# Kernel tuning notes

Measured on AMD Instinct MI355X. Metric: run time of the kernel, lower is better.

The kernel has to match this reference:

```python
import jax, jax.numpy as jnp
import numpy as np

B, C, T = 512, 256, 256
E, K, G = 8, 5, 8
EPS = 1e-5


def setup_inputs() -> dict:
    key = jax.random.key(0)
    k1, k2, k3, k4 = jax.random.split(key, 4)
    x = jax.random.normal(k1, (B, C, T), dtype=jnp.float32)
    use_expert_i = jax.random.randint(k2, (B,), 0, E, dtype=jnp.int32)
    # per-expert Conv1d params: weight [E, Cout, Cin, K], bias [E, Cout]
    W = jax.random.normal(k3, (E, C, C, K), dtype=jnp.float32) * 0.05
    b = jax.random.normal(k4, (E, C), dtype=jnp.float32) * 0.05
    # per-expert GroupNorm affine params (torch default init: gamma=1, beta=0)
    gamma = jnp.ones((E, C), dtype=jnp.float32)
    beta = jnp.zeros((E, C), dtype=jnp.float32)
    return {"x": x, "use_expert_i": use_expert_i, "W": W, "b": b,
            "gamma": gamma, "beta": beta}


def _mish(y):
    return y * jnp.tanh(jax.nn.softplus(y))


def reference(x, use_expert_i, W, b, gamma, beta):
    # Top-1 one-hot routing => weight is exactly 1 for the selected expert, so
    # output[b] = Mish(GroupNorm(Conv1d_{e_b}(x[b]))). Gather per-sample params
    # instead of looping over experts (same math, vectorized).
    pad = K // 2
    Wb = W[use_expert_i]        # [B, Cout, Cin, K]
    bb = b[use_expert_i]        # [B, Cout]
    gb = gamma[use_expert_i]    # [B, Cout]
    betab = beta[use_expert_i]  # [B, Cout]

    def per_sample_conv(xi, wi, bi):
        # xi: [Cin, T], wi: [Cout, Cin, K] -> [Cout, T] ('same' padding)
        y = jax.lax.conv_general_dilated(xi[None], wi, window_strides=(1,),
                                         padding=[(pad, pad)])[0]
        return y + bi[:, None]

    y = jax.vmap(per_sample_conv)(x, Wb, bb)  # [B, C, T]

    # GroupNorm: normalize over (channels-in-group, length) per sample
    yg = y.reshape(B, G, C // G, T)
    mu = jnp.mean(yg, axis=(2, 3), keepdims=True)
    var = jnp.var(yg, axis=(2, 3), keepdims=True)
    yn = ((yg - mu) * jax.lax.rsqrt(var + EPS)).reshape(B, C, T)
    yn = yn * gb[:, :, None] + betab[:, :, None]
    return _mish(yn)
```

## Files before the change

kernel.cpp:

```cpp
#include <hip/hip_runtime.h>
#include <cmath>

constexpr int Bn = 512, Cn = 256, Tn = 256, En = 8;
constexpr float EPSf = 1e-5f;

using bf16x8 = __attribute__((ext_vector_type(8))) short;
using f32x4  = __attribute__((ext_vector_type(4))) float;

__device__ __forceinline__ ushort f2bf(float f) {
    uint u = __builtin_bit_cast(uint, f);
    uint r = u + 0x7FFFu + ((u >> 16) & 1u);
    return (ushort)(r >> 16);
}

__global__ __launch_bounds__(256)
void wconv_kernel(const float* __restrict__ Wf, ushort* __restrict__ Wws) {
    int idx = blockIdx.x * 256 + threadIdx.x;
    const float* src = Wf + (size_t)idx * 5;
    int ci = idx & 255, co = (idx >> 8) & 255, e = idx >> 16;
#pragma unroll
    for (int k = 0; k < 5; ++k)
        Wws[(((size_t)(e * 5 + k) * 256 + co) << 8) + ci] = f2bf(src[k]);
}

__global__ __launch_bounds__(256)
void xpose_kernel(const float* __restrict__ x, ushort* __restrict__ xT) {
    const int id = blockIdx.x;
    const int b  = id >> 5;
    const int cc = (id >> 3) & 3, tc = id & 7;
    const int ci0 = cc * 64, t0 = tc * 32;
    const int tid = threadIdx.x;

    __shared__ float ls[64][33];

    const int tl = tid & 31;
#pragma unroll
    for (int jj = 0; jj < 8; ++jj) {
        const int cil = (tid >> 5) * 8 + jj;
        ls[cil][tl] = x[((size_t)(b * 256 + ci0 + cil)) * 256 + t0 + tl];
    }
    __syncthreads();

    const int ciw = tid & 63;
#pragma unroll
    for (int jj = 0; jj < 8; ++jj) {
        const int tw = (tid >> 6) * 8 + jj;
        xT[((size_t)(b * 256 + t0 + tw)) * 256 + ci0 + ciw] = f2bf(ls[ciw][tw]);
    }
}

template<int MODE>
__global__ __launch_bounds__(256, 3)
void conv_gn_mish(const float* __restrict__ x, const ushort* __restrict__ xTw,
                  const int* __restrict__ expert,
                  const float* __restrict__ Wf, const ushort* __restrict__ Wws,
                  const float* __restrict__ bias, const float* __restrict__ gamma,
                  const float* __restrict__ beta, float* __restrict__ out)
{
    const int id = blockIdx.x;
    const int wg = (id & 7) * 256 + (id >> 3);
    const int b  = wg >> 2;
    const int gp = wg & 3;
    const int cb = gp * 64;
    const int e  = __builtin_amdgcn_readfirstlane(expert[b]);

    const int tid = threadIdx.x;
    const int w = tid >> 6, l = tid & 63, q = l >> 4, r = l & 15;

    __shared__ ushort xT[2][260 * 40];
    __shared__ float red[4][4];

    f32x4 acc[4][4];
#pragma unroll
    for (int m = 0; m < 4; ++m)
#pragma unroll
        for (int n = 0; n < 4; ++n) acc[m][n] = f32x4{0.f, 0.f, 0.f, 0.f};

    if (tid < 8) {
        const int bf = tid >> 2, rr = tid & 3;
        const int row = (rr < 2) ? rr : (256 + rr);
#pragma unroll
        for (int i = 0; i < 10; ++i)
            *reinterpret_cast<uint2*>(&xT[bf][row * 40 + i * 4]) = make_uint2(0u, 0u);
    }

    bf16x8 g[4];
    float v[4][8];

#define STAGE_LOAD(CI0) {                                                    \
        if (MODE == 2) {                                                     \
            const ushort* xb = xTw + ((size_t)b * 256) * 256 + (CI0) + w * 8;\
            _Pragma("unroll")                                                \
            for (int tt = 0; tt < 4; ++tt)                                   \
                g[tt] = *reinterpret_cast<const bf16x8*>(                    \
                    xb + (size_t)(tt * 64 + l) * 256);                       \
        } else {                                                             \
            const float* xb = x + ((size_t)b * Cn + (CI0) + w * 8) * Tn;     \
            _Pragma("unroll")                                                \
            for (int tt = 0; tt < 4; ++tt) {                                 \
                const int t = tt * 64 + l;                                   \
                _Pragma("unroll")                                            \
                for (int rr = 0; rr < 8; ++rr) v[tt][rr] = xb[rr * Tn + t];  \
            }                                                                \
        }                                                                    \
    }
#define STAGE_WRITE(BUF) {                                                   \
        ushort* dst = xT[BUF];                                               \
        if (MODE == 2) {                                                     \
            _Pragma("unroll")                                                \
            for (int tt = 0; tt < 4; ++tt)                                   \
                *reinterpret_cast<bf16x8*>(                                  \
                    &dst[(tt * 64 + l + 2) * 40 + w * 8]) = g[tt];           \
        } else {                                                             \
            _Pragma("unroll")                                                \
            for (int tt = 0; tt < 4; ++tt) {                                 \
                const int t = tt * 64 + l;                                   \
                uint p0 = (uint)f2bf(v[tt][0]) | ((uint)f2bf(v[tt][1]) << 16); \
                uint p1 = (uint)f2bf(v[tt][2]) | ((uint)f2bf(v[tt][3]) << 16); \
                uint p2 = (uint)f2bf(v[tt][4]) | ((uint)f2bf(v[tt][5]) << 16); \
                uint p3 = (uint)f2bf(v[tt][6]) | ((uint)f2bf(v[tt][7]) << 16); \
                *reinterpret_cast<uint2*>(&dst[(t + 2) * 40 + w * 8])     = make_uint2(p0, p1); \
                *reinterpret_cast<uint2*>(&dst[(t + 2) * 40 + w * 8 + 4]) = make_uint2(p2, p3); \
            }                                                                \
        }                                                                    \
    }

    STAGE_LOAD(0);
    STAGE_WRITE(0);
    STAGE_LOAD(32);
    __syncthreads();

#pragma unroll 1
    for (int ct = 0; ct < 8; ++ct) {
        if (ct < 7) {
            STAGE_WRITE((ct + 1) & 1);
            if (ct < 6) STAGE_LOAD((ct + 2) * 32);
        }
        const int ci0 = ct * 32;
        const ushort* src = xT[ct & 1];

#pragma unroll
        for (int k = 0; k < 5; ++k) {
            bf16x8 A[4];
#pragma unroll
            for (int m = 0; m < 4; ++m) {
                if (MODE >= 1) {
                    A[m] = *reinterpret_cast<const bf16x8*>(
                        Wws + (((size_t)((e * 5 + k) * 256 + cb + m * 16 + r)) << 8)
                            + ci0 + q * 8);
                } else {
                    bf16x8 a;
#pragma unroll
                    for (int j = 0; j < 8; ++j)
                        a[j] = (short)f2bf(
                            Wf[((size_t)(e * 256 + cb + m * 16 + r) * 256
                                + ci0 + q * 8 + j) * 5 + k]);
                    A[m] = a;
                }
            }
#pragma unroll
            for (int n = 0; n < 4; ++n) {
                const bf16x8 Bf = *reinterpret_cast<const bf16x8*>(
                    &src[(w * 64 + n * 16 + r + k) * 40 + q * 8]);
#pragma unroll
                for (int m = 0; m < 4; ++m)
                    acc[m][n] = __builtin_amdgcn_mfma_f32_16x16x32_bf16(
                        A[m], Bf, acc[m][n], 0, 0, 0);
            }
        }
        __syncthreads();
    }
#undef STAGE_LOAD
#undef STAGE_WRITE

    float s1a = 0.f, s2a = 0.f, s1b = 0.f, s2b = 0.f;
#pragma unroll
    for (int m = 0; m < 4; ++m) {
#pragma unroll
        for (int i = 0; i < 4; ++i) {
            const float bv = bias[e * Cn + cb + m * 16 + q * 4 + i];
#pragma unroll
            for (int n = 0; n < 4; ++n) {
                const float val = acc[m][n][i] + bv;
                acc[m][n][i] = val;
                if (m < 2) { s1a += val; s2a += val * val; }
                else       { s1b += val; s2b += val * val; }
            }
        }
    }
#pragma unroll
    for (int off = 32; off; off >>= 1) {
        s1a += __shfl_xor(s1a, off); s2a += __shfl_xor(s2a, off);
        s1b += __shfl_xor(s1b, off); s2b += __shfl_xor(s2b, off);
    }
    if (l == 0) { red[w][0] = s1a; red[w][1] = s2a; red[w][2] = s1b; red[w][3] = s2b; }
    __syncthreads();
    const float S1a = red[0][0] + red[1][0] + red[2][0] + red[3][0];
    const float S2a = red[0][1] + red[1][1] + red[2][1] + red[3][1];
    const float S1b = red[0][2] + red[1][2] + red[2][2] + red[3][2];
    const float S2b = red[0][3] + red[1][3] + red[2][3] + red[3][3];

    constexpr float invn = 1.0f / (32 * 256);
    const float mua = S1a * invn, mub = S1b * invn;
    const float rsa = rsqrtf(fmaf(-mua, mua, S2a * invn) + EPSf);
    const float rsb = rsqrtf(fmaf(-mub, mub, S2b * invn) + EPSf);

#pragma unroll
    for (int m = 0; m < 4; ++m) {
        const float mu = (m < 2) ? mua : mub;
        const float rs = (m < 2) ? rsa : rsb;
#pragma unroll
        for (int i = 0; i < 4; ++i) {
            const int co = cb + m * 16 + q * 4 + i;
            const float sc = gamma[e * Cn + co] * rs;
            const float sh = beta[e * Cn + co] - mu * sc;
            float* orow = out + ((size_t)(b * Cn + co)) * Tn + w * 64 + r;
#pragma unroll
            for (int n = 0; n < 4; ++n) {
                const float y = fmaf(acc[m][n][i], sc, sh);
                const float u  = __expf(y);
                const float t2 = u * (u + 2.f);
                const float ms = (y > 20.f) ? y : y * t2 / (t2 + 2.f);
                orow[n * 16] = ms;
            }
        }
    }
}

extern "C" void kernel_launch(void* const* d_in, const int* in_sizes, int n_in,
                              void* d_out, int out_size, void* d_ws, size_t ws_size,
                              hipStream_t stream) {
    const float* x      = (const float*)d_in[0];
    const int*   expert = (const int*)  d_in[1];
    const float* Wf     = (const float*)d_in[2];
    const float* bias   = (const float*)d_in[3];
    const float* gamma  = (const float*)d_in[4];
    const float* beta   = (const float*)d_in[5];
    float* out = (float*)d_out;

    const size_t WWS_BYTES = (size_t)En * 5 * 256 * 256 * 2;
    const size_t XT_BYTES  = (size_t)Bn * 256 * 256 * 2;

    ushort* Wws = (ushort*)d_ws;
    ushort* xTw = (ushort*)((char*)d_ws + WWS_BYTES);

    if (ws_size >= WWS_BYTES + XT_BYTES) {
        hipLaunchKernelGGL(wconv_kernel, dim3(2048), dim3(256), 0, stream, Wf, Wws);
        hipLaunchKernelGGL(xpose_kernel, dim3(16384), dim3(256), 0, stream, x, xTw);
        hipLaunchKernelGGL((conv_gn_mish<2>), dim3(2048), dim3(256), 0, stream,
                           x, xTw, expert, Wf, Wws, bias, gamma, beta, out);
    } else if (ws_size >= WWS_BYTES) {
        hipLaunchKernelGGL(wconv_kernel, dim3(2048), dim3(256), 0, stream, Wf, Wws);
        hipLaunchKernelGGL((conv_gn_mish<1>), dim3(2048), dim3(256), 0, stream,
                           x, nullptr, expert, Wf, Wws, bias, gamma, beta, out);
    } else {
        hipLaunchKernelGGL((conv_gn_mish<0>), dim3(2048), dim3(256), 0, stream,
                           x, nullptr, expert, Wf, nullptr, bias, gamma, beta, out);
    }
}
```

Baseline: 242.9 us.

## Give each wave a private LDS x tile with halo and drop block barriers

```diff
diff --git a/kernel.cpp b/kernel.cpp
--- a/kernel.cpp
+++ b/kernel.cpp
@@ -66,8 +66,9 @@
 
     const int tid = threadIdx.x;
     const int w = tid >> 6, l = tid & 63, q = l >> 4, r = l & 15;
-
-    __shared__ ushort xT[2][260 * 40];
+    const int tw = w * 64;
+
+    __shared__ ushort xw[4][2][68 * 40];
     __shared__ float red[4][4];
 
     f32x4 acc[4][4];
@@ -76,59 +77,46 @@
 #pragma unroll
         for (int n = 0; n < 4; ++n) acc[m][n] = f32x4{0.f, 0.f, 0.f, 0.f};
 
-    if (tid < 8) {
-        const int bf = tid >> 2, rr = tid & 3;
-        const int row = (rr < 2) ? rr : (256 + rr);
-#pragma unroll
-        for (int i = 0; i < 10; ++i)
-            *reinterpret_cast<uint2*>(&xT[bf][row * 40 + i * 4]) = make_uint2(0u, 0u);
-    }
-
-    bf16x8 g[4];
-    float v[4][8];
+    const int srow = l >> 2;
+    const int slot = l & 3;
+    const bf16x8 zv = {0, 0, 0, 0, 0, 0, 0, 0};
+    bf16x8 g[5];
 
 #define STAGE_LOAD(CI0) {                                                    \
-        if (MODE == 2) {                                                     \
-            const ushort* xb = xTw + ((size_t)b * 256) * 256 + (CI0) + w * 8;\
-            _Pragma("unroll")                                                \
-            for (int tt = 0; tt < 4; ++tt)                                   \
-                g[tt] = *reinterpret_cast<const bf16x8*>(                    \
-                    xb + (size_t)(tt * 64 + l) * 256);                       \
-        } else {                                                             \
-            const float* xb = x + ((size_t)b * Cn + (CI0) + w * 8) * Tn;     \
-            _Pragma("unroll")                                                \
-            for (int tt = 0; tt < 4; ++tt) {                                 \
-                const int t = tt * 64 + l;                                   \
-                _Pragma("unroll")                                            \
-                for (int rr = 0; rr < 8; ++rr) v[tt][rr] = xb[rr * Tn + t];  \
+        _Pragma("unroll")                                                    \
+        for (int j = 0; j < 5; ++j) {                                        \
+            const int row = j * 16 + srow;                                   \
+            const int t = tw - 2 + row;                                      \
+            const bool ok = (row < 68) && (t >= 0) && (t < Tn);              \
+            if (MODE == 2) {                                                 \
+                g[j] = ok ? *reinterpret_cast<const bf16x8*>(                \
+                    xTw + ((size_t)(b * 256 + t)) * 256 + (CI0) + slot * 8)  \
+                          : zv;                                              \
+            } else {                                                         \
+                bf16x8 a = zv;                                               \
+                if (ok) {                                                    \
+                    const float* xp = x + ((size_t)b * Cn + (CI0) + slot * 8) * Tn + t; \
+                    _Pragma("unroll")                                        \
+                    for (int jj = 0; jj < 8; ++jj)                           \
+                        a[jj] = (short)f2bf(xp[jj * Tn]);                    \
+                }                                                            \
+                g[j] = a;                                                    \
             }                                                                \
         }                                                                    \
     }
 #define STAGE_WRITE(BUF) {                                                   \
-        ushort* dst = xT[BUF];                                               \
-        if (MODE == 2) {                                                     \
-            _Pragma("unroll")                                                \
-            for (int tt = 0; tt < 4; ++tt)                                   \
-                *reinterpret_cast<bf16x8*>(                                  \
-                    &dst[(tt * 64 + l + 2) * 40 + w * 8]) = g[tt];           \
-        } else {                                                             \
-            _Pragma("unroll")                                                \
-            for (int tt = 0; tt < 4; ++tt) {                                 \
-                const int t = tt * 64 + l;                                   \
-                uint p0 = (uint)f2bf(v[tt][0]) | ((uint)f2bf(v[tt][1]) << 16); \
-                uint p1 = (uint)f2bf(v[tt][2]) | ((uint)f2bf(v[tt][3]) << 16); \
-                uint p2 = (uint)f2bf(v[tt][4]) | ((uint)f2bf(v[tt][5]) << 16); \
-                uint p3 = (uint)f2bf(v[tt][6]) | ((uint)f2bf(v[tt][7]) << 16); \
-                *reinterpret_cast<uint2*>(&dst[(t + 2) * 40 + w * 8])     = make_uint2(p0, p1); \
-                *reinterpret_cast<uint2*>(&dst[(t + 2) * 40 + w * 8 + 4]) = make_uint2(p2, p3); \
-            }                                                                \
+        ushort* dst = &xw[w][BUF][0];                                        \
+        _Pragma("unroll")                                                    \
+        for (int j = 0; j < 5; ++j) {                                        \
+            const int row = j * 16 + srow;                                   \
+            if (row < 68)                                                    \
+                *reinterpret_cast<bf16x8*>(dst + row * 40 + slot * 8) = g[j];\
         }                                                                    \
     }
 
     STAGE_LOAD(0);
     STAGE_WRITE(0);
     STAGE_LOAD(32);
-    __syncthreads();
 
 #pragma unroll 1
     for (int ct = 0; ct < 8; ++ct) {
@@ -137,7 +125,7 @@
             if (ct < 6) STAGE_LOAD((ct + 2) * 32);
         }
         const int ci0 = ct * 32;
-        const ushort* src = xT[ct & 1];
+        const ushort* src = &xw[w][ct & 1][0];
 
 #pragma unroll
         for (int k = 0; k < 5; ++k) {
@@ -161,14 +149,13 @@
 #pragma unroll
             for (int n = 0; n < 4; ++n) {
                 const bf16x8 Bf = *reinterpret_cast<const bf16x8*>(
-                    &src[(w * 64 + n * 16 + r + k) * 40 + q * 8]);
+                    &src[(n * 16 + r + k) * 40 + q * 8]);
 #pragma unroll
                 for (int m = 0; m < 4; ++m)
                     acc[m][n] = __builtin_amdgcn_mfma_f32_16x16x32_bf16(
                         A[m], Bf, acc[m][n], 0, 0, 0);
             }
         }
-        __syncthreads();
     }
 #undef STAGE_LOAD
 #undef STAGE_WRITE
@@ -214,7 +201,7 @@
             const int co = cb + m * 16 + q * 4 + i;
             const float sc = gamma[e * Cn + co] * rs;
             const float sh = beta[e * Cn + co] - mu * sc;
-            float* orow = out + ((size_t)(b * Cn + co)) * Tn + w * 64 + r;
+            float* orow = out + ((size_t)(b * Cn + co)) * Tn + tw + r;
 #pragma unroll
             for (int n = 0; n < 4; ++n) {
                 const float y = fmaf(acc[m][n][i], sc, sh);
```

New measurement: 225.3 us. 1.08x faster.
